# Optimization experiments

Measured on AMD Instinct MI355X. Metric: run time of the kernel, lower is better.

## Reference

```python
import jax, jax.numpy as jnp
import numpy as np

IN_CH = 256
OUT_CH = 256
STATE = 384
OUT_SEQ = 32
B_SZ = 8
SEQ = 512


def setup_inputs() -> dict:
    key = jax.random.key(0)
    ks = jax.random.split(key, 8)
    rmin, rmax, max_phase = 0.0, 1.0, 6.283
    u1 = jax.random.uniform(ks[0], (STATE,))
    u2 = jax.random.uniform(ks[1], (STATE,))
    # standard LRU stable-ring initialization
    nu_log = jnp.log(-0.5 * jnp.log(u1 * (rmax + rmin) * (rmax - rmin) + rmin ** 2))
    theta_log = jnp.log(max_phase * u2)
    lam_mod = jnp.exp(-jnp.exp(nu_log))
    gamma_log = jnp.log(jnp.sqrt(1.0 - lam_mod ** 2))
    B_re = jax.random.normal(ks[2], (STATE, IN_CH)) / np.sqrt(2 * IN_CH)
    B_im = jax.random.normal(ks[3], (STATE, IN_CH)) / np.sqrt(2 * IN_CH)
    C_re = jax.random.normal(ks[4], (OUT_CH, STATE)) / np.sqrt(STATE)
    C_im = jax.random.normal(ks[5], (OUT_CH, STATE)) / np.sqrt(STATE)
    D = jax.random.normal(ks[6], (OUT_CH, IN_CH)) / np.sqrt(IN_CH)
    x = jax.random.normal(ks[7], (B_SZ, SEQ, IN_CH))
    return dict(x=x, nu_log=nu_log, theta_log=theta_log, gamma_log=gamma_log,
                B_re=B_re, B_im=B_im, C_re=C_re, C_im=C_im, D=D)


def _lru(x, h_re, h_im, nu_log, theta_log, gamma_log, B_re, B_im, C_re, C_im, D):
    """One LRU pass over a full sequence. x: [B,S,C]. h_*: [B,N] initial complex state.
    Diagonal complex recurrence h_t = Lambda*h_{t-1} + gamma*(B x_t); y_t = Re(C h_t) + D x_t."""
    lam_mod = jnp.exp(-jnp.exp(nu_log))              # |Lambda| in (0,1)
    lre = lam_mod * jnp.cos(jnp.exp(theta_log))      # [N]
    lim = lam_mod * jnp.sin(jnp.exp(theta_log))
    gamma = jnp.exp(gamma_log)
    # input projection for whole sequence (complex, split into re/im)
    u_re = gamma * jnp.einsum('bsc,nc->bsn', x, B_re)  # [B,S,N]
    u_im = gamma * jnp.einsum('bsc,nc->bsn', x, B_im)

    def step(h, u):
        hre, him = h
        ur, ui = u
        nre = lre * hre - lim * him + ur
        nim = lre * him + lim * hre + ui
        return (nre, nim), (nre, nim)

    (h_re, h_im), (hs_re, hs_im) = jax.lax.scan(
        step, (h_re, h_im),
        (jnp.swapaxes(u_re, 0, 1), jnp.swapaxes(u_im, 0, 1)))  # scan over S
    hs_re = jnp.swapaxes(hs_re, 0, 1)  # [B,S,N]
    hs_im = jnp.swapaxes(hs_im, 0, 1)
    y = (jnp.einsum('bsn,on->bso', hs_re, C_re)
         - jnp.einsum('bsn,on->bso', hs_im, C_im)
         + jnp.einsum('bsc,oc->bso', x, D))
    return y, h_re, h_im


def reference(x, nu_log, theta_log, gamma_log, B_re, B_im, C_re, C_im, D):
    bsz = x.shape[0]
    h_re = jnp.zeros((bsz, STATE), x.dtype)   # state=None on first call -> zeros
    h_im = jnp.zeros((bsz, STATE), x.dtype)
    outs = []
    for _ in range(OUT_SEQ):
        x, h_re, h_im = _lru(x, h_re, h_im, nu_log, theta_log, gamma_log,
                             B_re, B_im, C_re, C_im, D)
        outs.append(x[:, -1:])
    return jnp.concatenate(outs, axis=-2)  # [B, OUT_SEQ, OUT_CH]
```

## Files before the change

kernel.cpp:

```cpp
#include <hip/hip_runtime.h>
#include <hip/hip_bf16.h>
#include <math.h>

typedef unsigned short u16;
typedef __attribute__((ext_vector_type(8))) short bf16x8;
typedef __attribute__((ext_vector_type(4))) float f32x4;

#define IN_CH   256
#define STATE   384
#define OUT_SEQ 32
#define B_SZ    8
#define SEQ     512
#define M_ROWS  4096
#define NJ      768

#define PS_WB  (NJ*IN_CH)
#define PS_WC  (IN_CH*NJ)
#define PS_WD  (IN_CH*IN_CH)
#define PS_Z   ((size_t)M_ROWS*NJ)
#define PS_X   ((size_t)M_ROWS*IN_CH)

static constexpr size_t B_U   = 0;
static constexpr size_t B_Z   = B_U  + 8*(size_t)M_ROWS*IN_CH*4;
static constexpr size_t B_XA  = B_Z  + 3*(size_t)M_ROWS*NJ*2;
static constexpr size_t B_XB  = B_XA + 3*(size_t)M_ROWS*IN_CH*2;
static constexpr size_t B_WB  = B_XB + 3*(size_t)M_ROWS*IN_CH*2;
static constexpr size_t B_WC  = B_WB + 3*(size_t)PS_WB*2;
static constexpr size_t B_WD  = B_WC + 3*(size_t)PS_WC*2;
static constexpr size_t B_LAM = B_WD + 3*(size_t)PS_WD*2;
static constexpr size_t B_HC  = B_LAM + 2*768*4;

__device__ __forceinline__ u16 f2b(float v) {
    __hip_bfloat16 h = __float2bfloat16(v);
    return *(u16*)&h;
}
__device__ __forceinline__ float b2f(u16 u) {
    __hip_bfloat16 h = *(__hip_bfloat16*)&u;
    return __bfloat162float(h);
}
__device__ __forceinline__ void split3(float v, u16& a, u16& b, u16& c) {
    a = f2b(v);  float r1 = v  - b2f(a);
    b = f2b(r1); float r2 = r1 - b2f(b);
    c = f2b(r2);
}

__device__ __forceinline__ size_t a_idx(int row, int k, int NKC) {
    return ((size_t)(((row >> 5)*NKC + (k >> 5))*2 + ((k >> 4) & 1))*2 + ((k >> 3) & 1))*256
           + (size_t)(row & 31)*8 + (k & 7);
}

__device__ __forceinline__ void frag_decode(int r, int& t32, int& h, int& hi5,
                                            int& lo5, int& e) {
    t32 = r >> 10; int r2 = r & 1023;
    h = r2 >> 9;   int r3 = r2 & 511;
    hi5 = r3 >> 8; int r4 = r3 & 255;
    lo5 = r4 >> 3; e = r4 & 7;
}

__global__ void prep_lam_hc(const float* __restrict__ nu_log,
                            const float* __restrict__ th_log,
                            float* __restrict__ lam, float* __restrict__ lam16,
                            float* __restrict__ hc0) {
    int n = threadIdx.x;
    if (n < STATE) {
        float lm = expf(-expf(nu_log[n]));
        float th = expf(th_log[n]);
        float ar = lm * cosf(th), ai = lm * sinf(th);
        lam[2*n] = ar; lam[2*n+1] = ai;
        float pr = ar, pi = ai;
#pragma unroll
        for (int i = 0; i < 4; ++i) {
            float nr = pr*pr - pi*pi, ni = 2.f*pr*pi;
            pr = nr; pi = ni;
        }
        lam16[2*n] = pr; lam16[2*n+1] = pi;
    }
    for (int i = threadIdx.x; i < B_SZ*NJ; i += blockDim.x) hc0[i] = 0.f;
}

__global__ void prep_wb(const float* __restrict__ B_re, const float* __restrict__ B_im,
                        const float* __restrict__ gamma_log, u16* __restrict__ W) {
    int idx = blockIdx.x*blockDim.x + threadIdx.x;
    int c32 = idx >> 13, r = idx & 8191;
    int t32,h,hi5,lo5,e; frag_decode(r, t32,h,hi5,lo5,e);
    int j = c32*32 + lo5;
    int k = t32*32 + (2*h + hi5)*8 + e;
    int n = j >> 1;
    float g = expf(gamma_log[n]);
    float v = g * ((j & 1) ? B_im[n*IN_CH + k] : B_re[n*IN_CH + k]);
    u16 a,b,cc; split3(v,a,b,cc);
    W[idx] = a; W[idx + PS_WB] = b; W[idx + 2*PS_WB] = cc;
}

__global__ void prep_wcd(const float* __restrict__ C_re, const float* __restrict__ C_im,
                         const float* __restrict__ D,
                         u16* __restrict__ WC, u16* __restrict__ WD) {
    int idx = blockIdx.x*blockDim.x + threadIdx.x;
    if (idx < PS_WC) {
        int c32 = idx / 24576, r = idx % 24576;
        int t32,h,hi5,lo5,e; frag_decode(r, t32,h,hi5,lo5,e);
        int o = c32*32 + lo5;
        int j = t32*32 + (2*h + hi5)*8 + e;
        int n = j >> 1;
        float v = (j & 1) ? -C_im[o*STATE + n] : C_re[o*STATE + n];
        u16 a,b,c; split3(v,a,b,c);
        WC[idx] = a; WC[idx + PS_WC] = b; WC[idx + 2*PS_WC] = c;
    } else {
        int q = idx - PS_WC;
        int c32 = q >> 13, r = q & 8191;
        int t32,h,hi5,lo5,e; frag_decode(r, t32,h,hi5,lo5,e);
        int o = c32*32 + lo5;
        int c = t32*32 + (2*h + hi5)*8 + e;
        float v = D[o*IN_CH + c];
        u16 a,b,cc; split3(v,a,b,cc);
        WD[q] = a; WD[q + PS_WD] = b; WD[q + 2*PS_WD] = cc;
    }
}

__global__ void prep_x(const float* __restrict__ x,
                       u16* __restrict__ X1, u16* __restrict__ X2, u16* __restrict__ X3) {
    int idx = blockIdx.x*blockDim.x + threadIdx.x;
    int row = idx >> 8, k = idx & 255;
    u16 a,b,c; split3(x[idx],a,b,c);
    size_t o = a_idx(row, k, 8);
    X1[o] = a; X2[o] = b; X3[o] = c;
}

__device__ __constant__ const int cPI[6] = {0,0,1,0,1,2};
__device__ __constant__ const int cPJ[6] = {0,1,0,2,1,0};

struct G1P { const u16* A[3]; };

__global__ __launch_bounds__(512, 2)
void front_k(G1P ga, const u16* __restrict__ WBp,
             u16* __restrict__ Z1, u16* __restrict__ Z2, u16* __restrict__ Z3,
             const float* __restrict__ lam, const float* __restrict__ lam16,
             const float2* __restrict__ HcIn, float2* __restrict__ HcOut) {
    __shared__ __align__(16) float Ls[512*34];
    __shared__ float2 car[32][16];
    __shared__ float2 hp[32][16];
    const int tid = threadIdx.x, lane = tid & 63, w = tid >> 6;
    const int b = blockIdx.x & 7, jt = blockIdx.x >> 3;
    const int l15 = lane & 15, q = lane >> 4;
    const int hb = q >> 1, hi5q = q & 1;

    f32x4 acc[4][2];
#pragma unroll
    for (int i = 0; i < 4; ++i)
#pragma unroll
        for (int n16 = 0; n16 < 2; ++n16) acc[i][n16] = 0.f;

    bf16x8 av[2][4][3], bv[2][2][3];
    auto loadA = [&](int buf, int kc) {
#pragma unroll
        for (int p = 0; p < 3; ++p)
#pragma unroll
            for (int i = 0; i < 4; ++i) {
                int m16 = i*8 + w;
                int row32 = b*16 + (m16 >> 1);
                int rin = ((m16 & 1) << 4) + l15;
                av[buf][i][p] = *(const bf16x8*)(ga.A[p]
                    + ((((size_t)(row32*8 + kc)*2 + hb)*2 + hi5q) << 8) + rin*8);
            }
    };
    auto loadB = [&](int buf, int kc) {
#pragma unroll
        for (int p = 0; p < 3; ++p)
#pragma unroll
            for (int n16 = 0; n16 < 2; ++n16)
                bv[buf][n16][p] = *(const bf16x8*)(WBp + (size_t)p*PS_WB
                    + ((((size_t)(jt*8 + kc)*2 + hb)*2 + hi5q) << 8) + (n16*16 + l15)*8);
    };

    loadA(0, 0); loadB(0, 0);
    loadA(1, 1); loadB(1, 1);
#pragma unroll
    for (int kc = 0; kc < 8; ++kc) {
        const int cb = kc & 1;
#pragma unroll
        for (int t6 = 0; t6 < 6; ++t6)
#pragma unroll
            for (int i = 0; i < 4; ++i)
#pragma unroll
                for (int n16 = 0; n16 < 2; ++n16)
                    acc[i][n16] = __builtin_amdgcn_mfma_f32_16x16x32_bf16(
                        av[cb][i][cPI[t6]], bv[cb][n16][cPJ[t6]], acc[i][n16], 0, 0, 0);
        if (kc + 2 < 8) { loadA(cb, kc + 2); loadB(cb, kc + 2); }
    }

#pragma unroll
    for (int i = 0; i < 4; ++i) {
        int m16 = i*8 + w;
#pragma unroll
        for (int n16 = 0; n16 < 2; ++n16)
#pragma unroll
            for (int r = 0; r < 4; ++r) {
                int s = m16*16 + q*4 + r;
                int jl = n16*16 + l15;
                Ls[s*34 + jl] = acc[i][n16][r];
            }
    }
    __syncthreads();

    {
        int st = tid & 15, ch = tid >> 4;
        int n = jt*16 + st;
        float lre = lam[2*n], lim = lam[2*n+1];
        float hr = 0.f, hm = 0.f;
#pragma unroll
        for (int t = 0; t < 16; ++t) {
            int s = ch*16 + t;
            float2 u = *(const float2*)&Ls[s*34 + 2*st];
            float nr = fmaf(lre, hr, fmaf(-lim, hm, u.x));
            float nm = fmaf(lre, hm, fmaf( lim, hr, u.y));
            hr = nr; hm = nm;
        }
        car[ch][st] = make_float2(hr, hm);
    }
    __syncthreads();

    if (tid < 16) {
        int st = tid, n = jt*16 + st;
        float l16r = lam16[2*n], l16i = lam16[2*n+1];
        float2 hh = HcIn[(size_t)b*STATE + n];
        hp[0][st] = hh;
#pragma unroll
        for (int ch = 1; ch < 32; ++ch) {
            float2 cj = car[ch-1][st];
            float nr = fmaf(l16r, hh.x, fmaf(-l16i, hh.y, cj.x));
            float ni = fmaf(l16r, hh.y, fmaf( l16i, hh.x, cj.y));
            hh.x = nr; hh.y = ni;
            hp[ch][st] = hh;
        }
    }
    __syncthreads();

    {
        int st = tid & 15, ch = tid >> 4;
        int n = jt*16 + st;
        float lre = lam[2*n], lim = lam[2*n+1];
        float2 hh = hp[ch][st];
        int j0 = jt*32 + 2*st;
#pragma unroll
        for (int t = 0; t < 16; ++t) {
            int s = ch*16 + t;
            float2 u = *(const float2*)&Ls[s*34 + 2*st];
            float nr = fmaf(lre, hh.x, fmaf(-lim, hh.y, u.x));
            float ni = fmaf(lre, hh.y, fmaf( lim, hh.x, u.y));
            hh.x = nr; hh.y = ni;
            u16 a1,a2,a3, c1,c2,c3;
            split3(nr, a1,a2,a3);
            split3(ni, c1,c2,c3);
            size_t zo = a_idx(b*512 + s, j0, 24);
            ushort2 t2;
            t2.x = a1; t2.y = c1; *(ushort2*)(Z1 + zo) = t2;
            t2.x = a2; t2.y = c2; *(ushort2*)(Z2 + zo) = t2;
            t2.x = a3; t2.y = c3; *(ushort2*)(Z3 + zo) = t2;
        }
        if (ch == 31) HcOut[(size_t)b*STATE + n] = hh;
    }
}

struct G2P {
    const u16* Z[3]; const u16* X[3]; const u16* WC; const u16* WD;
    u16* O1; u16* O2; u16* O3; float* outp; int iter;
};

__global__ __launch_bounds__(512, 2)
void gemm2_k(G2P g) {
    __shared__ __align__(16) float Lred[64*64];
    const int tid = threadIdx.x, lane = tid & 63, w = tid >> 6;
    const int kg = w >> 2, wq = w & 3;
    const int wr = wq & 1, wcq = wq >> 1;
    const int m0 = blockIdx.x*64, n0 = blockIdx.y*64;
    const int hi5 = lane >> 5, lo5 = lane & 31;
    const int c32 = (n0 >> 5) + wcq;
    const int m32 = blockIdx.x*2 + wr;
    const int cbase = kg*16;

    typedef __attribute__((ext_vector_type(16))) float f32x16_t;
    f32x16_t accv;
#pragma unroll
    for (int i = 0; i < 16; ++i) accv[i] = 0.f;

    auto aptr = [&](int p, int c, int h) -> const u16* {
        if (c < 24)
            return g.Z[p] + ((((size_t)(m32*24 + c)*2 + h)*2 + hi5) << 8) + lo5*8;
        return g.X[p] + ((((size_t)(m32*8 + (c - 24))*2 + h)*2 + hi5) << 8) + lo5*8;
    };
    auto bptr = [&](int p, int c, int h) -> const u16* {
        if (c < 24)
            return g.WC + (size_t)p*PS_WC
                   + ((((size_t)(c32*24 + c)*2 + h)*2 + hi5) << 8) + lo5*8;
        return g.WD + (size_t)p*PS_WD
               + ((((size_t)(c32*8 + (c - 24))*2 + h)*2 + hi5) << 8) + lo5*8;
    };

    bf16x8 bwin[3][4][2];
    auto loadB = [&](int wnd, int tlo, int thi) {
#pragma unroll
        for (int p = 0; p < 3; ++p)
#pragma unroll
            for (int t = 0; t < 4; ++t) {
                if (t < tlo || t >= thi) continue;
#pragma unroll
                for (int h = 0; h < 2; ++h)
                    bwin[p][t][h] = *(const bf16x8*)bptr(p, cbase + wnd*4 + t, h);
            }
    };
    bf16x8 av[2][3][2];
    auto loadA = [&](int buf, int t) {
#pragma unroll
        for (int p = 0; p < 3; ++p)
#pragma unroll
            for (int h = 0; h < 2; ++h)
                av[buf][p][h] = *(const bf16x8*)aptr(p, cbase + t, h);
    };

    loadA(0, 0);
    loadB(0, 0, 4);
    loadA(1, 1);
#pragma unroll
    for (int t = 0; t < 16; ++t) {
        if ((t & 3) == 2 && t < 12) loadB((t >> 2) + 1, 0, 2);
        const int cb = t & 1;
        const int tw = t & 3;
#pragma unroll
        for (int t6 = 0; t6 < 6; ++t6)
            accv = __builtin_amdgcn_mfma_f32_32x32x16_bf16(
                av[cb][cPI[t6]][0], bwin[cPJ[t6]][tw][0],
                __builtin_amdgcn_mfma_f32_32x32x16_bf16(
                    av[cb][cPI[t6]][1], bwin[cPJ[t6]][tw][1], accv, 0, 0, 0),
                0, 0, 0);
        if ((t & 3) == 3 && t < 12) loadB((t >> 2) + 1, 2, 4);
        if (t + 2 < 16) loadA(cb, t + 2);
    }

    if (kg == 1) {
#pragma unroll
        for (int reg = 0; reg < 16; ++reg) {
            int rl = wr*32 + (reg & 3) + 8*(reg >> 2) + 4*hi5;
            int cl = wcq*32 + lo5;
            Lred[rl*64 + cl] = accv[reg];
        }
    }
    __syncthreads();
    if (kg == 0) {
#pragma unroll
        for (int reg = 0; reg < 16; ++reg) {
            int rl = wr*32 + (reg & 3) + 8*(reg >> 2) + 4*hi5;
            int cl = wcq*32 + lo5;
            float v = accv[reg] + Lred[rl*64 + cl];
            int row = m0 + rl, col = n0 + cl;
            u16 a,b,c; split3(v, a,b,c);
            size_t o = a_idx(row, col, 8);
            g.O1[o] = a; g.O2[o] = b; g.O3[o] = c;
            if ((row & (SEQ-1)) == SEQ-1)
                g.outp[(size_t)((row >> 9)*OUT_SEQ + g.iter)*IN_CH + col] = v;
        }
    }
}

extern "C" void kernel_launch(void* const* d_in, const int* in_sizes, int n_in,
                              void* d_out, int out_size, void* d_ws, size_t ws_size,
                              hipStream_t stream) {
    const float* x_in      = (const float*)d_in[0];
    const float* nu_log    = (const float*)d_in[1];
    const float* theta_log = (const float*)d_in[2];
    const float* gamma_log = (const float*)d_in[3];
    const float* B_re      = (const float*)d_in[4];
    const float* B_im      = (const float*)d_in[5];
    const float* C_re      = (const float*)d_in[6];
    const float* C_im      = (const float*)d_in[7];
    const float* D         = (const float*)d_in[8];
    float* out = (float*)d_out;

    char* ws = (char*)d_ws;
    u16* Z1 = (u16*)(ws + B_Z);
    u16* Z2 = Z1 + PS_Z;
    u16* Z3 = Z2 + PS_Z;
    u16* XA1 = (u16*)(ws + B_XA);
    u16* XA2 = XA1 + PS_X;
    u16* XA3 = XA2 + PS_X;
    u16* XB1 = (u16*)(ws + B_XB);
    u16* XB2 = XB1 + PS_X;
    u16* XB3 = XB2 + PS_X;
    u16* WB  = (u16*)(ws + B_WB);
    u16* WCt = (u16*)(ws + B_WC);
    u16* WDt = (u16*)(ws + B_WD);
    float* lam   = (float*)(ws + B_LAM);
    float* lam16 = lam + 768;
    float2* Hc0  = (float2*)(ws + B_HC);
    float2* Hc1  = Hc0 + (size_t)B_SZ*STATE;

    prep_lam_hc<<<1, 384, 0, stream>>>(nu_log, theta_log, lam, lam16, (float*)Hc0);
    prep_wb<<<PS_WB/256, 256, 0, stream>>>(B_re, B_im, gamma_log, WB);
    prep_wcd<<<(PS_WC + PS_WD)/256, 256, 0, stream>>>(C_re, C_im, D, WCt, WDt);
    prep_x<<<(M_ROWS*IN_CH)/256, 256, 0, stream>>>(x_in, XA1, XA2, XA3);

    for (int it = 0; it < OUT_SEQ; ++it) {
        u16* Xc[3]; u16* Xn[3];
        if (it & 1) { Xc[0]=XB1; Xc[1]=XB2; Xc[2]=XB3; Xn[0]=XA1; Xn[1]=XA2; Xn[2]=XA3; }
        else        { Xc[0]=XA1; Xc[1]=XA2; Xc[2]=XA3; Xn[0]=XB1; Xn[1]=XB2; Xn[2]=XB3; }
        float2* Hin  = (it & 1) ? Hc1 : Hc0;
        float2* Hout = (it & 1) ? Hc0 : Hc1;

        G1P g1;
        for (int p = 0; p < 3; ++p) g1.A[p] = Xc[p];
        front_k<<<192, 512, 0, stream>>>(
            g1, WB, Z1, Z2, Z3, lam, lam16, Hin, Hout);

        G2P g2;
        g2.Z[0]=Z1; g2.Z[1]=Z2; g2.Z[2]=Z3;
        g2.X[0]=Xc[0]; g2.X[1]=Xc[1]; g2.X[2]=Xc[2];
        g2.WC = WCt; g2.WD = WDt;
        g2.O1 = Xn[0]; g2.O2 = Xn[1]; g2.O3 = Xn[2];
        g2.outp = out; g2.iter = it;
        gemm2_k<<<dim3(M_ROWS/64, IN_CH/64), 512, 0, stream>>>(g2);
    }
}
```

Measured before the change: 1.330 ms.

## Move D-projection GEMM into front kernel and parallelize chunk carry scan

Adds 64 extra blocks to front_k that compute the x·D skip product into an fp32 workspace buffer P. These blocks run alongside the B-projection and scan blocks, so gemm2_k only reduces over the state dimension (K shrinks from 32 to 24 chunks) and adds P in its epilogue. It also replaces the serial 32-step inter-chunk carry propagation, done by 16 threads, with a wave-level Kogge-Stone scan over complex affine maps using shuffles. The cost is an extra fp32 round trip through global memory for P and some redundant complex multiplies in the scan.

```diff
diff --git a/kernel.cpp b/kernel.cpp
--- a/kernel.cpp
+++ b/kernel.cpp
@@ -5,6 +5,7 @@
 typedef unsigned short u16;
 typedef __attribute__((ext_vector_type(8))) short bf16x8;
 typedef __attribute__((ext_vector_type(4))) float f32x4;
+typedef __attribute__((ext_vector_type(16))) float f32x16;
 
 #define IN_CH   256
 #define STATE   384
@@ -132,17 +133,75 @@
 struct G1P { const u16* A[3]; };
 
 __global__ __launch_bounds__(512, 2)
-void front_k(G1P ga, const u16* __restrict__ WBp,
+void front_k(G1P ga, const u16* __restrict__ WBp, const u16* __restrict__ WDp,
              u16* __restrict__ Z1, u16* __restrict__ Z2, u16* __restrict__ Z3,
+             float* __restrict__ P,
              const float* __restrict__ lam, const float* __restrict__ lam16,
              const float2* __restrict__ HcIn, float2* __restrict__ HcOut) {
     __shared__ __align__(16) float Ls[512*34];
     __shared__ float2 car[32][16];
     __shared__ float2 hp[32][16];
     const int tid = threadIdx.x, lane = tid & 63, w = tid >> 6;
-    const int b = blockIdx.x & 7, jt = blockIdx.x >> 3;
     const int l15 = lane & 15, q = lane >> 4;
     const int hb = q >> 1, hi5q = q & 1;
+    const int hi5 = lane >> 5, lo5 = lane & 31;
+
+    if (blockIdx.x >= 192) {
+        const int mt = blockIdx.x - 192;
+        const int wr = w & 1, wc = w >> 1;
+        const int m32 = mt*2 + wr;
+        f32x16 acc[2];
+#pragma unroll
+        for (int cj = 0; cj < 2; ++cj)
+#pragma unroll
+            for (int i = 0; i < 16; ++i) acc[cj][i] = 0.f;
+
+        bf16x8 av[2][3][2], bv[2][2][3][2];
+        auto loadA = [&](int buf, int kc) {
+#pragma unroll
+            for (int p = 0; p < 3; ++p)
+#pragma unroll
+                for (int h = 0; h < 2; ++h)
+                    av[buf][p][h] = *(const bf16x8*)(ga.A[p]
+                        + ((((size_t)(m32*8 + kc)*2 + h)*2 + hi5) << 8) + lo5*8);
+        };
+        auto loadB = [&](int buf, int kc) {
+#pragma unroll
+            for (int cj = 0; cj < 2; ++cj)
+#pragma unroll
+                for (int p = 0; p < 3; ++p)
+#pragma unroll
+                    for (int h = 0; h < 2; ++h)
+                        bv[buf][cj][p][h] = *(const bf16x8*)(WDp + (size_t)p*PS_WD
+                            + ((((size_t)((wc*2 + cj)*8 + kc)*2 + h)*2 + hi5) << 8) + lo5*8);
+        };
+        loadA(0, 0); loadB(0, 0);
+        loadA(1, 1); loadB(1, 1);
+#pragma unroll
+        for (int kc = 0; kc < 8; ++kc) {
+            const int cb = kc & 1;
+#pragma unroll
+            for (int t6 = 0; t6 < 6; ++t6)
+#pragma unroll
+                for (int cj = 0; cj < 2; ++cj)
+#pragma unroll
+                    for (int h = 0; h < 2; ++h)
+                        acc[cj] = __builtin_amdgcn_mfma_f32_32x32x16_bf16(
+                            av[cb][cPI[t6]][h], bv[cb][cj][cPJ[t6]][h], acc[cj], 0, 0, 0);
+            if (kc + 2 < 8) { loadA(cb, kc + 2); loadB(cb, kc + 2); }
+        }
+#pragma unroll
+        for (int cj = 0; cj < 2; ++cj)
+#pragma unroll
+            for (int reg = 0; reg < 16; ++reg) {
+                int row = mt*64 + wr*32 + (reg & 3) + 8*(reg >> 2) + 4*hi5;
+                int col = wc*64 + cj*32 + lo5;
+                P[(size_t)row*IN_CH + col] = acc[cj][reg];
+            }
+        return;
+    }
+
+    const int b = blockIdx.x & 7, jt = blockIdx.x >> 3;
 
     f32x4 acc[4][2];
 #pragma unroll
@@ -219,19 +278,41 @@
     }
     __syncthreads();
 
-    if (tid < 16) {
-        int st = tid, n = jt*16 + st;
-        float l16r = lam16[2*n], l16i = lam16[2*n+1];
-        float2 hh = HcIn[(size_t)b*STATE + n];
-        hp[0][st] = hh;
-#pragma unroll
-        for (int ch = 1; ch < 32; ++ch) {
-            float2 cj = car[ch-1][st];
-            float nr = fmaf(l16r, hh.x, fmaf(-l16i, hh.y, cj.x));
-            float ni = fmaf(l16r, hh.y, fmaf( l16i, hh.x, cj.y));
-            hh.x = nr; hh.y = ni;
-            hp[ch][st] = hh;
-        }
+    {
+        int st2 = 2*w + hi5, ch2 = lane & 31;
+        int n = jt*16 + st2;
+        float2 e = car[ch2][st2];
+        float Ar = lam16[2*n], Ai = lam16[2*n+1];
+        float Br = e.x, Bi = e.y;
+#pragma unroll
+        for (int d = 1; d < 32; d <<= 1) {
+            int src = (lane & 32) | ((lane - d) & 31);
+            float pAr = __shfl(Ar, src), pAi = __shfl(Ai, src);
+            float pBr = __shfl(Br, src), pBi = __shfl(Bi, src);
+            if (ch2 >= d) {
+                float nAr = Ar*pAr - Ai*pAi;
+                float nAi = Ar*pAi + Ai*pAr;
+                float nBr = fmaf(Ar, pBr, fmaf(-Ai, pBi, Br));
+                float nBi = fmaf(Ar, pBi, fmaf( Ai, pBr, Bi));
+                Ar = nAr; Ai = nAi; Br = nBr; Bi = nBi;
+            }
+        }
+        float2 s0 = HcIn[(size_t)b*STATE + n];
+        if (ch2 == 31) {
+            float fr = fmaf(Ar, s0.x, fmaf(-Ai, s0.y, Br));
+            float fi = fmaf(Ar, s0.y, fmaf( Ai, s0.x, Bi));
+            HcOut[(size_t)b*STATE + n] = make_float2(fr, fi);
+        }
+        int srcp = (lane & 32) | ((lane - 1) & 31);
+        float eAr = __shfl(Ar, srcp), eAi = __shfl(Ai, srcp);
+        float eBr = __shfl(Br, srcp), eBi = __shfl(Bi, srcp);
+        float sr, si;
+        if (ch2 == 0) { sr = s0.x; si = s0.y; }
+        else {
+            sr = fmaf(eAr, s0.x, fmaf(-eAi, s0.y, eBr));
+            si = fmaf(eAr, s0.y, fmaf( eAi, s0.x, eBi));
+        }
+        hp[ch2][st2] = make_float2(sr, si);
     }
     __syncthreads();
 
@@ -257,12 +338,11 @@
             t2.x = a2; t2.y = c2; *(ushort2*)(Z2 + zo) = t2;
             t2.x = a3; t2.y = c3; *(ushort2*)(Z3 + zo) = t2;
         }
-        if (ch == 31) HcOut[(size_t)b*STATE + n] = hh;
     }
 }
 
 struct G2P {
-    const u16* Z[3]; const u16* X[3]; const u16* WC; const u16* WD;
+    const u16* Z[3]; const u16* WC; const float* P;
     u16* O1; u16* O2; u16* O3; float* outp; int iter;
 };
 
@@ -276,24 +356,18 @@
     const int hi5 = lane >> 5, lo5 = lane & 31;
     const int c32 = (n0 >> 5) + wcq;
     const int m32 = blockIdx.x*2 + wr;
-    const int cbase = kg*16;
-
-    typedef __attribute__((ext_vector_type(16))) float f32x16_t;
-    f32x16_t accv;
+    const int cbase = kg*12;
+
+    f32x16 accv;
 #pragma unroll
     for (int i = 0; i < 16; ++i) accv[i] = 0.f;
 
     auto aptr = [&](int p, int c, int h) -> const u16* {
-        if (c < 24)
-            return g.Z[p] + ((((size_t)(m32*24 + c)*2 + h)*2 + hi5) << 8) + lo5*8;
-        return g.X[p] + ((((size_t)(m32*8 + (c - 24))*2 + h)*2 + hi5) << 8) + lo5*8;
+        return g.Z[p] + ((((size_t)(m32*24 + c)*2 + h)*2 + hi5) << 8) + lo5*8;
     };
     auto bptr = [&](int p, int c, int h) -> const u16* {
-        if (c < 24)
-            return g.WC + (size_t)p*PS_WC
-                   + ((((size_t)(c32*24 + c)*2 + h)*2 + hi5) << 8) + lo5*8;
-        return g.WD + (size_t)p*PS_WD
-               + ((((size_t)(c32*8 + (c - 24))*2 + h)*2 + hi5) << 8) + lo5*8;
+        return g.WC + (size_t)p*PS_WC
+               + ((((size_t)(c32*24 + c)*2 + h)*2 + hi5) << 8) + lo5*8;
     };
 
     bf16x8 bwin[3][4][2];
@@ -321,8 +395,8 @@
     loadB(0, 0, 4);
     loadA(1, 1);
 #pragma unroll
-    for (int t = 0; t < 16; ++t) {
-        if ((t & 3) == 2 && t < 12) loadB((t >> 2) + 1, 0, 2);
+    for (int t = 0; t < 12; ++t) {
+        if ((t & 3) == 2 && t < 8) loadB((t >> 2) + 1, 0, 2);
         const int cb = t & 1;
         const int tw = t & 3;
 #pragma unroll
@@ -332,8 +406,8 @@
                 __builtin_amdgcn_mfma_f32_32x32x16_bf16(
                     av[cb][cPI[t6]][1], bwin[cPJ[t6]][tw][1], accv, 0, 0, 0),
                 0, 0, 0);
-        if ((t & 3) == 3 && t < 12) loadB((t >> 2) + 1, 2, 4);
-        if (t + 2 < 16) loadA(cb, t + 2);
+        if ((t & 3) == 3 && t < 8) loadB((t >> 2) + 1, 2, 4);
+        if (t + 2 < 12) loadA(cb, t + 2);
     }
 
     if (kg == 1) {
@@ -350,8 +424,8 @@
         for (int reg = 0; reg < 16; ++reg) {
             int rl = wr*32 + (reg & 3) + 8*(reg >> 2) + 4*hi5;
             int cl = wcq*32 + lo5;
-            float v = accv[reg] + Lred[rl*64 + cl];
             int row = m0 + rl, col = n0 + cl;
+            float v = accv[reg] + Lred[rl*64 + cl] + g.P[(size_t)row*IN_CH + col];
             u16 a,b,c; split3(v, a,b,c);
             size_t o = a_idx(row, col, 8);
             g.O1[o] = a; g.O2[o] = b; g.O3[o] = c;
@@ -376,6 +450,7 @@
     float* out = (float*)d_out;
 
     char* ws = (char*)d_ws;
+    float* P = (float*)(ws + B_U);
     u16* Z1 = (u16*)(ws + B_Z);
     u16* Z2 = Z1 + PS_Z;
     u16* Z3 = Z2 + PS_Z;
@@ -407,13 +482,12 @@
 
         G1P g1;
         for (int p = 0; p < 3; ++p) g1.A[p] = Xc[p];
-        front_k<<<192, 512, 0, stream>>>(
-            g1, WB, Z1, Z2, Z3, lam, lam16, Hin, Hout);
+        front_k<<<256, 512, 0, stream>>>(
+            g1, WB, WDt, Z1, Z2, Z3, P, lam, lam16, Hin, Hout);
 
         G2P g2;
         g2.Z[0]=Z1; g2.Z[1]=Z2; g2.Z[2]=Z3;
-        g2.X[0]=Xc[0]; g2.X[1]=Xc[1]; g2.X[2]=Xc[2];
-        g2.WC = WCt; g2.WD = WDt;
+        g2.WC = WCt; g2.P = P;
         g2.O1 = Xn[0]; g2.O2 = Xn[1]; g2.O3 = Xn[2];
         g2.outp = out; g2.iter = it;
         gemm2_k<<<dim3(M_ROWS/64, IN_CH/64), 512, 0, stream>>>(g2);
```

Measured after the change: 1.262 ms. -5.2%, faster.
